# Kernel tuning notes

Measured on AMD Instinct MI355X. Metric: run time of the kernel, lower is better.

The kernel has to match this reference:

```python
import jax, jax.numpy as jnp
import numpy as np

D_MODEL = 1024
N_HEADS = 16
HEAD_DIM = D_MODEL // N_HEADS
B, L = 2, 2048


def setup_inputs() -> dict:
    key = jax.random.key(0)
    ks = jax.random.split(key, 11)
    s = 1.0 / np.sqrt(D_MODEL)
    inp = {
        'query': jax.random.normal(ks[0], (B, L, D_MODEL), dtype=jnp.float32),
        'key': jax.random.normal(ks[1], (B, L, D_MODEL), dtype=jnp.float32),
        'value': jax.random.normal(ks[2], (B, L, D_MODEL), dtype=jnp.float32),
        'Wq_w': jax.random.normal(ks[3], (D_MODEL, D_MODEL), dtype=jnp.float32) * s,
        'Wq_b': jnp.zeros((D_MODEL,), dtype=jnp.float32),
        'Wk_w': jax.random.normal(ks[4], (D_MODEL, D_MODEL), dtype=jnp.float32) * s,
        'Wk_b': jnp.zeros((D_MODEL,), dtype=jnp.float32),
        'Wv_w': jax.random.normal(ks[5], (D_MODEL, D_MODEL), dtype=jnp.float32) * s,
        'Wv_b': jnp.zeros((D_MODEL,), dtype=jnp.float32),
        'Wo_w': jax.random.normal(ks[6], (D_MODEL, D_MODEL), dtype=jnp.float32) * s,
        'Wo_b': jnp.zeros((D_MODEL,), dtype=jnp.float32),
    }
    return inp


def reference(query, key, value, Wq_w, Wq_b, Wk_w, Wk_b, Wv_w, Wv_b, Wo_w, Wo_b):
    b = query.shape[0]
    # torch Linear: y = x @ W^T + b
    Q = query @ Wq_w.T + Wq_b
    K = key @ Wk_w.T + Wk_b
    V = value @ Wv_w.T + Wv_b
    # [B, L, D] -> [B, H, L, hd]
    def split_heads(x):
        return x.reshape(b, -1, N_HEADS, HEAD_DIM).transpose(0, 2, 1, 3)
    Qh, Kh, Vh = split_heads(Q), split_heads(K), split_heads(V)
    scale = 1.0 / jnp.sqrt(jnp.float32(HEAD_DIM))
    # energy: [B, H, Lq, Lk]
    energy = jnp.einsum('bhqd,bhkd->bhqk', Qh, Kh) * scale
    # NOTE: original code applies softmax over dim=1 (the HEADS axis) — faithful reproduction
    attn = jax.nn.softmax(energy, axis=1)
    out = jnp.einsum('bhqk,bhkd->bhqd', attn, Vh)  # [B, H, Lq, hd]
    out = out.transpose(0, 2, 1, 3).reshape(b, -1, D_MODEL)
    return out @ Wo_w.T + Wo_b
```

## Files before the change

kernel.cpp:

```cpp
#include <hip/hip_runtime.h>
#include <hip/hip_bf16.h>
#include <hip/hip_fp16.h>

#define DM 1024
#define NH 16
#define HD 64
#define LL 2048

typedef __attribute__((ext_vector_type(8))) short bf16x8;
typedef __attribute__((ext_vector_type(4))) float f32x4;

#define MFMA16(a,b,c) __builtin_amdgcn_mfma_f32_16x16x32_bf16((a),(b),(c),0,0,0)

#define GL16(g, l) __builtin_amdgcn_global_load_lds( \
    (const __attribute__((address_space(1))) unsigned int*)(g), \
    (__attribute__((address_space(3))) unsigned int*)(l), 16, 0, 0)

__device__ __forceinline__ ushort f2bf(float f) {
  union { float f; unsigned int u; } v; v.f = f;
  unsigned int u = v.u + 0x7fffu + ((v.u >> 16) & 1u);
  return (ushort)(u >> 16);
}

__global__ __launch_bounds__(256) void cvt7(const float* __restrict__ s0, ushort* __restrict__ d0, int n0,
                                            const float* __restrict__ s1, ushort* __restrict__ d1, int n1,
                                            const float* __restrict__ s2, ushort* __restrict__ d2, int n2,
                                            const float* __restrict__ s3, ushort* __restrict__ d3, int n3,
                                            const float* __restrict__ s4, ushort* __restrict__ d4, int n4,
                                            const float* __restrict__ s5, ushort* __restrict__ d5, int n5,
                                            const float* __restrict__ s6, ushort* __restrict__ d6, int n6) {
  int i = (blockIdx.x * 256 + threadIdx.x) * 4;
  const float* s; ushort* d;
  if (i < n0) { s = s0; d = d0; }
  else if ((i -= n0) < n1) { s = s1; d = d1; }
  else if ((i -= n1) < n2) { s = s2; d = d2; }
  else if ((i -= n2) < n3) { s = s3; d = d3; }
  else if ((i -= n3) < n4) { s = s4; d = d4; }
  else if ((i -= n4) < n5) { s = s5; d = d5; }
  else if ((i -= n5) < n6) { s = s6; d = d6; }
  else return;
  float4 v = *(const float4*)(s + i);
  union { ushort u[4]; unsigned long long ll; } o;
  o.u[0] = f2bf(v.x); o.u[1] = f2bf(v.y); o.u[2] = f2bf(v.z); o.u[3] = f2bf(v.w);
  *(unsigned long long*)(d + i) = o.ll;
}

__global__ __launch_bounds__(256) void gemm_qkv(const ushort* __restrict__ qA, const ushort* __restrict__ qW,
                                                const float* __restrict__ qb, ushort* __restrict__ qO,
                                                const ushort* __restrict__ kA, const ushort* __restrict__ kW,
                                                const float* __restrict__ kb, ushort* __restrict__ kO,
                                                const ushort* __restrict__ vA, const ushort* __restrict__ vW,
                                                const float* __restrict__ vb, ushort* __restrict__ vO) {
  __shared__ ushort lA[2][128][64];
  __shared__ ushort lB[2][128][64];
  const int z = blockIdx.z;
  const ushort* Ab; const ushort* Wb; const float* bias; ushort* outp;
  float alpha; bool trans;
  if (z == 0)      { Ab = qA; Wb = qW; bias = qb; outp = qO; alpha = 0.125f; trans = false; }
  else if (z == 1) { Ab = kA; Wb = kW; bias = kb; outp = kO; alpha = 1.0f;   trans = false; }
  else             { Ab = vA; Wb = vW; bias = vb; outp = vO; alpha = 1.0f;   trans = true;  }

  const int m0 = blockIdx.x * 128, n0 = blockIdx.y * 128;
  const int t = threadIdx.x;
  const int w = t >> 6, lane = t & 63, lr = lane & 15, lg = lane >> 4;
  const int wm = (w >> 1) * 64, wn = (w & 1) * 64;
  const int lrow8 = lane >> 3;
  const int scol = ((lane & 7) ^ lrow8) * 8;

  f32x4 acc[4][4];
  #pragma unroll
  for (int i = 0; i < 4; ++i)
    #pragma unroll
    for (int j = 0; j < 4; ++j) acc[i][j] = (f32x4){0.f, 0.f, 0.f, 0.f};

  #pragma unroll
  for (int c = 0; c < 4; ++c) {
    GL16(Ab + (m0 + w * 32 + c * 8 + lrow8) * DM + scol, &lA[0][w * 32 + c * 8][0]);
    GL16(Wb + (n0 + w * 32 + c * 8 + lrow8) * DM + scol, &lB[0][w * 32 + c * 8][0]);
  }
  __syncthreads();

  int cur = 0;
  for (int k0 = 0; k0 < DM; k0 += 64) {
    if (k0 + 64 < DM) {
      #pragma unroll
      for (int c = 0; c < 4; ++c) {
        GL16(Ab + (m0 + w * 32 + c * 8 + lrow8) * DM + k0 + 64 + scol, &lA[cur ^ 1][w * 32 + c * 8][0]);
        GL16(Wb + (n0 + w * 32 + c * 8 + lrow8) * DM + k0 + 64 + scol, &lB[cur ^ 1][w * 32 + c * 8][0]);
      }
    }
    #pragma unroll
    for (int ks = 0; ks < 2; ++ks) {
      bf16x8 aF[4], bF[4];
      #pragma unroll
      for (int i = 0; i < 4; ++i)
        aF[i] = *(const bf16x8*)&lA[cur][wm + i * 16 + lr][(((ks * 4 + lg) ^ (lr & 7)) * 8)];
      #pragma unroll
      for (int j = 0; j < 4; ++j)
        bF[j] = *(const bf16x8*)&lB[cur][wn + j * 16 + lr][(((ks * 4 + lg) ^ (lr & 7)) * 8)];
      #pragma unroll
      for (int i = 0; i < 4; ++i)
        #pragma unroll
        for (int j = 0; j < 4; ++j)
          acc[i][j] = MFMA16(aF[i], bF[j], acc[i][j]);
    }
    __syncthreads();
    cur ^= 1;
  }

  #pragma unroll
  for (int i = 0; i < 4; ++i)
    #pragma unroll
    for (int j = 0; j < 4; ++j)
      #pragma unroll
      for (int r = 0; r < 4; ++r) {
        int m = m0 + wm + i * 16 + lg * 4 + r;
        int n = n0 + wn + j * 16 + lr;
        float v = (acc[i][j][r] + bias[n]) * alpha;
        int b = m >> 11, q = m & 2047, h = n >> 6, d = n & 63;
        if (!trans)
          outp[((b * NH + h) * LL + q) * HD + d] = f2bf(v);
        else
          outp[((b * NH + h) * HD + d) * LL + q] = f2bf(v);
      }
}

__global__ __launch_bounds__(256) void gemm_out(const ushort* __restrict__ Ab,
                                                const ushort* __restrict__ Wb,
                                                const float* __restrict__ bias,
                                                float* __restrict__ outf) {
  __shared__ ushort lA[2][64][64];
  __shared__ ushort lB[2][128][64];
  const int m0 = blockIdx.x * 64, n0 = blockIdx.y * 128;
  const int t = threadIdx.x;
  const int w = t >> 6, lane = t & 63, lr = lane & 15, lg = lane >> 4;
  const int wm = (w >> 1) * 32, wn = (w & 1) * 64;
  const int lrow8 = lane >> 3;
  const int scol = ((lane & 7) ^ lrow8) * 8;

  f32x4 acc[2][4];
  #pragma unroll
  for (int i = 0; i < 2; ++i)
    #pragma unroll
    for (int j = 0; j < 4; ++j) acc[i][j] = (f32x4){0.f, 0.f, 0.f, 0.f};

  #pragma unroll
  for (int c = 0; c < 2; ++c)
    GL16(Ab + (m0 + w * 16 + c * 8 + lrow8) * DM + scol, &lA[0][w * 16 + c * 8][0]);
  #pragma unroll
  for (int c = 0; c < 4; ++c)
    GL16(Wb + (n0 + w * 32 + c * 8 + lrow8) * DM + scol, &lB[0][w * 32 + c * 8][0]);
  __syncthreads();

  int cur = 0;
  for (int k0 = 0; k0 < DM; k0 += 64) {
    if (k0 + 64 < DM) {
      #pragma unroll
      for (int c = 0; c < 2; ++c)
        GL16(Ab + (m0 + w * 16 + c * 8 + lrow8) * DM + k0 + 64 + scol, &lA[cur ^ 1][w * 16 + c * 8][0]);
      #pragma unroll
      for (int c = 0; c < 4; ++c)
        GL16(Wb + (n0 + w * 32 + c * 8 + lrow8) * DM + k0 + 64 + scol, &lB[cur ^ 1][w * 32 + c * 8][0]);
    }
    #pragma unroll
    for (int ks = 0; ks < 2; ++ks) {
      bf16x8 aF[2], bF[4];
      #pragma unroll
      for (int i = 0; i < 2; ++i)
        aF[i] = *(const bf16x8*)&lA[cur][wm + i * 16 + lr][(((ks * 4 + lg) ^ (lr & 7)) * 8)];
      #pragma unroll
      for (int j = 0; j < 4; ++j)
        bF[j] = *(const bf16x8*)&lB[cur][wn + j * 16 + lr][(((ks * 4 + lg) ^ (lr & 7)) * 8)];
      #pragma unroll
      for (int i = 0; i < 2; ++i)
        #pragma unroll
        for (int j = 0; j < 4; ++j)
          acc[i][j] = MFMA16(aF[i], bF[j], acc[i][j]);
    }
    __syncthreads();
    cur ^= 1;
  }

  #pragma unroll
  for (int i = 0; i < 2; ++i)
    #pragma unroll
    for (int j = 0; j < 4; ++j)
      #pragma unroll
      for (int r = 0; r < 4; ++r) {
        int m = m0 + wm + i * 16 + lg * 4 + r;
        int n = n0 + wn + j * 16 + lr;
        outf[m * DM + n] = acc[i][j][r] + bias[n];
      }
}

__global__ __launch_bounds__(256) void pass_a_m(const ushort* __restrict__ Qh,
                                                const ushort* __restrict__ Kh,
                                                __half* __restrict__ rdenH) {
  __shared__ ushort lQ[2][128][64];
  __shared__ ushort lK[2][128][64];
  const int b = blockIdx.z, q0 = blockIdx.y * 128, k0 = blockIdx.x * 128;
  const int t = threadIdx.x, w = t >> 6, lane = t & 63, lr = lane & 15, lg = lane >> 4;
  const int lrow8 = lane >> 3;
  const int scol = ((lane & 7) ^ lrow8) * 8;

  f32x4 acc[2][8];
  #pragma unroll
  for (int i = 0; i < 2; ++i)
    #pragma unroll
    for (int j = 0; j < 8; ++j) acc[i][j] = (f32x4){0.f, 0.f, 0.f, 0.f};

  #pragma unroll
  for (int c = 0; c < 4; ++c) {
    GL16(Qh + ((b * NH) * LL + q0 + w * 32 + c * 8 + lrow8) * HD + scol, &lQ[0][w * 32 + c * 8][0]);
    GL16(Kh + ((b * NH) * LL + k0 + w * 32 + c * 8 + lrow8) * HD + scol, &lK[0][w * 32 + c * 8][0]);
  }
  __syncthreads();

  int cur = 0;
  for (int h = 0; h < NH; ++h) {
    if (h + 1 < NH) {
      #pragma unroll
      for (int c = 0; c < 4; ++c) {
        GL16(Qh + ((b * NH + h + 1) * LL + q0 + w * 32 + c * 8 + lrow8) * HD + scol, &lQ[cur ^ 1][w * 32 + c * 8][0]);
        GL16(Kh + ((b * NH + h + 1) * LL + k0 + w * 32 + c * 8 + lrow8) * HD + scol, &lK[cur ^ 1][w * 32 + c * 8][0]);
      }
    }
    #pragma unroll
    for (int i = 0; i < 2; ++i) {
      int qrow = w * 32 + i * 16 + lr;
      bf16x8 a0 = *(const bf16x8*)&lQ[cur][qrow][((lg ^ (lr & 7)) * 8)];
      bf16x8 a1 = *(const bf16x8*)&lQ[cur][qrow][(((4 + lg) ^ (lr & 7)) * 8)];
      #pragma unroll
      for (int j = 0; j < 8; ++j) {
        int krow = j * 16 + lr;
        bf16x8 b0 = *(const bf16x8*)&lK[cur][krow][((lg ^ (lr & 7)) * 8)];
        bf16x8 b1 = *(const bf16x8*)&lK[cur][krow][(((4 + lg) ^ (lr & 7)) * 8)];
        f32x4 e = {0.f, 0.f, 0.f, 0.f};
        e = MFMA16(b0, a0, e);
        e = MFMA16(b1, a1, e);
        #pragma unroll
        for (int r = 0; r < 4; ++r) acc[i][j][r] += __expf(e[r]);
      }
    }
    __syncthreads();
    cur ^= 1;
  }

  #pragma unroll
  for (int i = 0; i < 2; ++i)
    #pragma unroll
    for (int j = 0; j < 8; ++j) {
      int q = q0 + w * 32 + i * 16 + lr;
      int k = k0 + j * 16 + lg * 4;
      union { __half2 h2[2]; uint2 u; } pk;
      pk.h2[0] = __floats2half2_rn(__builtin_amdgcn_rcpf(acc[i][j][0]),
                                   __builtin_amdgcn_rcpf(acc[i][j][1]));
      pk.h2[1] = __floats2half2_rn(__builtin_amdgcn_rcpf(acc[i][j][2]),
                                   __builtin_amdgcn_rcpf(acc[i][j][3]));
      *(uint2*)&rdenH[(size_t)(b * LL + q) * LL + k] = pk.u;
    }
}

#define PB_BODY(PH)                                                              \
  {                                                                              \
    const int T = tt + PH;                                                       \
    const int k0 = T * 64;                                                       \
    uint2 rdN[4];                                                                \
    if (T + 1 < 32) {                                                            \
      GL16(Kh + (bh * LL + k0 + 64 + w * 8 + lrow8) * HD + scol,                 \
           &lK[PH ^ 1][w * 8][0]);                                               \
      GL16(Vt + (bh * HD + w * 8 + lrow8) * LL + k0 + 64 + scol,                 \
           &lV[PH ^ 1][w * 8][0]);                                               \
      _Pragma("unroll")                                                          \
      for (int j = 0; j < 4; ++j)                                                \
        rdN[j] = *(const uint2*)(rrow + k0 + 64 + j * 16 + lg * 4);              \
    }                                                                            \
    __builtin_amdgcn_s_setprio(1);                                               \
    if (T > 0) {                                                                 \
      bf16x8 aP0 = *(const bf16x8*)&U.p[w][lr][lg * 8];                          \
      bf16x8 aP1 = *(const bf16x8*)&U.p[w][lr][32 + lg * 8];                     \
      _Pragma("unroll")                                                          \
      for (int j = 0; j < 4; ++j) {                                              \
        accO[j] = MFMA16(aP0, vF0[j], accO[j]);                                  \
        accO[j] = MFMA16(aP1, vF1[j], accO[j]);                                  \
      }                                                                          \
    }                                                                            \
    f32x4 e[4];                                                                  \
    _Pragma("unroll")                                                            \
    for (int j = 0; j < 4; ++j) {                                                \
      int krow = j * 16 + lr;                                                    \
      bf16x8 kf0 = *(const bf16x8*)&lK[PH][krow][((lg ^ (lr & 7)) * 8)];         \
      bf16x8 kf1 = *(const bf16x8*)&lK[PH][krow][(((4 + lg) ^ (lr & 7)) * 8)];   \
      e[j] = (f32x4){0.f, 0.f, 0.f, 0.f};                                        \
      e[j] = MFMA16(kf0, aQ0, e[j]);                                             \
      e[j] = MFMA16(kf1, aQ1, e[j]);                                             \
    }                                                                            \
    __builtin_amdgcn_s_setprio(0);                                               \
    _Pragma("unroll")                                                            \
    for (int j = 0; j < 4; ++j) {                                                \
      int vrow = j * 16 + lr;                                                    \
      vF0[j] = *(const bf16x8*)&lV[PH][vrow][((lg ^ (lr & 7)) * 8)];             \
      vF1[j] = *(const bf16x8*)&lV[PH][vrow][(((4 + lg) ^ (lr & 7)) * 8)];       \
    }                                                                            \
    _Pragma("unroll")                                                            \
    for (int j = 0; j < 4; ++j) {                                                \
      float2 f0 = __half22float2(*reinterpret_cast<const __half2*>(&rdC[j].x));  \
      float2 f1 = __half22float2(*reinterpret_cast<const __half2*>(&rdC[j].y));  \
      union { __hip_bfloat162 b2[2]; uint2 u; } pk;                              \
      pk.b2[0] = __float22bfloat162_rn(make_float2(__expf(e[j][0]) * f0.x,       \
                                                   __expf(e[j][1]) * f0.y));     \
      pk.b2[1] = __float22bfloat162_rn(make_float2(__expf(e[j][2]) * f1.x,       \
                                                   __expf(e[j][3]) * f1.y));     \
      *(uint2*)&U.p[w][lr][j * 16 + lg * 4] = pk.u;                              \
    }                                                                            \
    if (T + 1 < 32) {                                                            \
      _Pragma("unroll")                                                          \
      for (int j = 0; j < 4; ++j) rdC[j] = rdN[j];                               \
    }                                                                            \
    __syncthreads();                                                             \
  }

__global__ __launch_bounds__(512, 4) void pass_b_m(const ushort* __restrict__ Qh,
                                                   const ushort* __restrict__ Kh,
                                                   const ushort* __restrict__ Vt,
                                                   const __half* __restrict__ rdenH,
                                                   ushort* __restrict__ AO) {
  __shared__ union UQP { ushort q[128][64]; ushort p[8][16][72]; } U;
  __shared__ ushort lK[2][64][64];
  __shared__ ushort lV[2][64][64];
  const int fid = blockIdx.x + 16 * (blockIdx.y + NH * blockIdx.z);
  const int nid = (fid & 7) * 64 + (fid >> 3);
  const int q0 = (nid & 15) * 128;
  const int h  = (nid >> 4) & 15;
  const int b  = nid >> 8;
  const int t = threadIdx.x, w = t >> 6, lane = t & 63, lr = lane & 15, lg = lane >> 4;
  const int lrow8 = lane >> 3;
  const int scol = ((lane & 7) ^ lrow8) * 8;
  const int bh = b * NH + h;

  #pragma unroll
  for (int u = 0; u < 2; ++u) {
    int c = u * 512 + t;
    int row = c >> 3, col = (c & 7) * 8;
    *(bf16x8*)&U.q[row][col] = *(const bf16x8*)&Qh[(bh * LL + q0 + row) * HD + col];
  }
  GL16(Kh + (bh * LL + w * 8 + lrow8) * HD + scol, &lK[0][w * 8][0]);
  GL16(Vt + (bh * HD + w * 8 + lrow8) * LL + scol, &lV[0][w * 8][0]);
  const int qg = q0 + w * 16 + lr;
  const __half* rrow = rdenH + (size_t)(b * LL + qg) * LL;
  uint2 rdC[4];
  #pragma unroll
  for (int j = 0; j < 4; ++j) rdC[j] = *(const uint2*)(rrow + j * 16 + lg * 4);
  __syncthreads();

  bf16x8 aQ0 = *(const bf16x8*)&U.q[w * 16 + lr][lg * 8];
  bf16x8 aQ1 = *(const bf16x8*)&U.q[w * 16 + lr][32 + lg * 8];
  __syncthreads();

  f32x4 accO[4];
  #pragma unroll
  for (int j = 0; j < 4; ++j) accO[j] = (f32x4){0.f, 0.f, 0.f, 0.f};
  bf16x8 vF0[4], vF1[4];

  for (int tt = 0; tt < 32; tt += 2) {
    PB_BODY(0)
    PB_BODY(1)
  }

  {
    bf16x8 aP0 = *(const bf16x8*)&U.p[w][lr][lg * 8];
    bf16x8 aP1 = *(const bf16x8*)&U.p[w][lr][32 + lg * 8];
    #pragma unroll
    for (int j = 0; j < 4; ++j) {
      accO[j] = MFMA16(aP0, vF0[j], accO[j]);
      accO[j] = MFMA16(aP1, vF1[j], accO[j]);
    }
  }

  #pragma unroll
  for (int j = 0; j < 4; ++j)
    #pragma unroll
    for (int r = 0; r < 4; ++r) {
      int q = q0 + w * 16 + lg * 4 + r;
      int d = j * 16 + lr;
      AO[(b * LL + q) * DM + h * HD + d] = f2bf(accO[j][r]);
    }
}

extern "C" void kernel_launch(void* const* d_in, const int* in_sizes, int n_in,
                              void* d_out, int out_size, void* d_ws, size_t ws_size,
                              hipStream_t stream) {
  const float* query = (const float*)d_in[0];
  const float* key   = (const float*)d_in[1];
  const float* value = (const float*)d_in[2];
  const float* Wq_w  = (const float*)d_in[3];
  const float* Wq_b  = (const float*)d_in[4];
  const float* Wk_w  = (const float*)d_in[5];
  const float* Wk_b  = (const float*)d_in[6];
  const float* Wv_w  = (const float*)d_in[7];
  const float* Wv_b  = (const float*)d_in[8];
  const float* Wo_w  = (const float*)d_in[9];
  const float* Wo_b  = (const float*)d_in[10];

  char* ws = (char*)d_ws;
  char* dob = (char*)d_out;
  ushort* Qh  = (ushort*)(ws);
  ushort* Kh  = (ushort*)(ws + (8u  << 20));
  ushort* Vt  = (ushort*)(ws + (16u << 20));
  ushort* AO  = (ushort*)(ws + (24u << 20));
  ushort* qbf = (ushort*)(ws + (32u << 20));
  ushort* kbf = (ushort*)(ws + (40u << 20));
  ushort* Wob = (ushort*)(ws + (48u << 20));
  ushort* vbf = (ushort*)(dob);
  ushort* Wqb = (ushort*)(dob + (8u  << 20));
  ushort* Wkb = (ushort*)(dob + (10u << 20));
  ushort* Wvb = (ushort*)(dob + (12u << 20));
  __half* rdn = (__half*)d_out;

  const int NA = 2 * LL * DM;
  const int NW = DM * DM;

  cvt7<<<(3 * NA + 4 * NW) / 1024, 256, 0, stream>>>(
      query, qbf, NA, key, kbf, NA, value, vbf, NA,
      Wq_w, Wqb, NW, Wk_w, Wkb, NW, Wv_w, Wvb, NW, Wo_w, Wob, NW);

  gemm_qkv<<<dim3(32, 8, 3), 256, 0, stream>>>(qbf, Wqb, Wq_b, Qh,
                                               kbf, Wkb, Wk_b, Kh,
                                               vbf, Wvb, Wv_b, Vt);

  pass_a_m<<<dim3(16, 16, 2), 256, 0, stream>>>(Qh, Kh, rdn);
  pass_b_m<<<dim3(16, NH, 2), 512, 0, stream>>>(Qh, Kh, Vt, rdn, AO);

  gemm_out<<<dim3(64, 8), 256, 0, stream>>>(AO, Wob, Wo_b, (float*)d_out);
}
```

Before: 192.2 us.

## Read K/V fragments directly from global memory, dropping LDS double-buffer pipeline

The P·V pass kernel stops staging K and V tiles in LDS through async global_load_lds double buffering with barriers. Each wave now loads its Q, K and V MFMA fragments straight from global memory and relies on cache, keeping LDS only for the per-wave P transpose. This removes the barriers and shared-memory staging, but every wave re-reads the same K/V tiles and loses the prefetch overlap. The occupancy hint in launch_bounds is dropped. The P store and reload now go through LDS without any sync, which is presumably safe only because each wave reads just the rows it wrote itself.

```diff
diff --git a/kernel.cpp b/kernel.cpp
--- a/kernel.cpp
+++ b/kernel.cpp
@@ -261,119 +261,63 @@
     }
 }
 
-#define PB_BODY(PH)                                                              \
-  {                                                                              \
-    const int T = tt + PH;                                                       \
-    const int k0 = T * 64;                                                       \
-    uint2 rdN[4];                                                                \
-    if (T + 1 < 32) {                                                            \
-      GL16(Kh + (bh * LL + k0 + 64 + w * 8 + lrow8) * HD + scol,                 \
-           &lK[PH ^ 1][w * 8][0]);                                               \
-      GL16(Vt + (bh * HD + w * 8 + lrow8) * LL + k0 + 64 + scol,                 \
-           &lV[PH ^ 1][w * 8][0]);                                               \
-      _Pragma("unroll")                                                          \
-      for (int j = 0; j < 4; ++j)                                                \
-        rdN[j] = *(const uint2*)(rrow + k0 + 64 + j * 16 + lg * 4);              \
-    }                                                                            \
-    __builtin_amdgcn_s_setprio(1);                                               \
-    if (T > 0) {                                                                 \
-      bf16x8 aP0 = *(const bf16x8*)&U.p[w][lr][lg * 8];                          \
-      bf16x8 aP1 = *(const bf16x8*)&U.p[w][lr][32 + lg * 8];                     \
-      _Pragma("unroll")                                                          \
-      for (int j = 0; j < 4; ++j) {                                              \
-        accO[j] = MFMA16(aP0, vF0[j], accO[j]);                                  \
-        accO[j] = MFMA16(aP1, vF1[j], accO[j]);                                  \
-      }                                                                          \
-    }                                                                            \
-    f32x4 e[4];                                                                  \
-    _Pragma("unroll")                                                            \
-    for (int j = 0; j < 4; ++j) {                                                \
-      int krow = j * 16 + lr;                                                    \
-      bf16x8 kf0 = *(const bf16x8*)&lK[PH][krow][((lg ^ (lr & 7)) * 8)];         \
-      bf16x8 kf1 = *(const bf16x8*)&lK[PH][krow][(((4 + lg) ^ (lr & 7)) * 8)];   \
-      e[j] = (f32x4){0.f, 0.f, 0.f, 0.f};                                        \
-      e[j] = MFMA16(kf0, aQ0, e[j]);                                             \
-      e[j] = MFMA16(kf1, aQ1, e[j]);                                             \
-    }                                                                            \
-    __builtin_amdgcn_s_setprio(0);                                               \
-    _Pragma("unroll")                                                            \
-    for (int j = 0; j < 4; ++j) {                                                \
-      int vrow = j * 16 + lr;                                                    \
-      vF0[j] = *(const bf16x8*)&lV[PH][vrow][((lg ^ (lr & 7)) * 8)];             \
-      vF1[j] = *(const bf16x8*)&lV[PH][vrow][(((4 + lg) ^ (lr & 7)) * 8)];       \
-    }                                                                            \
-    _Pragma("unroll")                                                            \
-    for (int j = 0; j < 4; ++j) {                                                \
-      float2 f0 = __half22float2(*reinterpret_cast<const __half2*>(&rdC[j].x));  \
-      float2 f1 = __half22float2(*reinterpret_cast<const __half2*>(&rdC[j].y));  \
-      union { __hip_bfloat162 b2[2]; uint2 u; } pk;                              \
-      pk.b2[0] = __float22bfloat162_rn(make_float2(__expf(e[j][0]) * f0.x,       \
-                                                   __expf(e[j][1]) * f0.y));     \
-      pk.b2[1] = __float22bfloat162_rn(make_float2(__expf(e[j][2]) * f1.x,       \
-                                                   __expf(e[j][3]) * f1.y));     \
-      *(uint2*)&U.p[w][lr][j * 16 + lg * 4] = pk.u;                              \
-    }                                                                            \
-    if (T + 1 < 32) {                                                            \
-      _Pragma("unroll")                                                          \
-      for (int j = 0; j < 4; ++j) rdC[j] = rdN[j];                               \
-    }                                                                            \
-    __syncthreads();                                                             \
-  }
-
-__global__ __launch_bounds__(512, 4) void pass_b_m(const ushort* __restrict__ Qh,
-                                                   const ushort* __restrict__ Kh,
-                                                   const ushort* __restrict__ Vt,
-                                                   const __half* __restrict__ rdenH,
-                                                   ushort* __restrict__ AO) {
-  __shared__ union UQP { ushort q[128][64]; ushort p[8][16][72]; } U;
-  __shared__ ushort lK[2][64][64];
-  __shared__ ushort lV[2][64][64];
+__global__ __launch_bounds__(512) void pass_b_m(const ushort* __restrict__ Qh,
+                                                const ushort* __restrict__ Kh,
+                                                const ushort* __restrict__ Vt,
+                                                const __half* __restrict__ rdenH,
+                                                ushort* __restrict__ AO) {
+  __shared__ ushort lP[8][16][72];
   const int fid = blockIdx.x + 16 * (blockIdx.y + NH * blockIdx.z);
   const int nid = (fid & 7) * 64 + (fid >> 3);
   const int q0 = (nid & 15) * 128;
   const int h  = (nid >> 4) & 15;
   const int b  = nid >> 8;
   const int t = threadIdx.x, w = t >> 6, lane = t & 63, lr = lane & 15, lg = lane >> 4;
-  const int lrow8 = lane >> 3;
-  const int scol = ((lane & 7) ^ lrow8) * 8;
   const int bh = b * NH + h;
-
-  #pragma unroll
-  for (int u = 0; u < 2; ++u) {
-    int c = u * 512 + t;
-    int row = c >> 3, col = (c & 7) * 8;
-    *(bf16x8*)&U.q[row][col] = *(const bf16x8*)&Qh[(bh * LL + q0 + row) * HD + col];
-  }
-  GL16(Kh + (bh * LL + w * 8 + lrow8) * HD + scol, &lK[0][w * 8][0]);
-  GL16(Vt + (bh * HD + w * 8 + lrow8) * LL + scol, &lV[0][w * 8][0]);
   const int qg = q0 + w * 16 + lr;
+
+  const ushort* qp = Qh + (size_t)(bh * LL + qg) * HD;
+  bf16x8 aQ0 = *(const bf16x8*)(qp + lg * 8);
+  bf16x8 aQ1 = *(const bf16x8*)(qp + 32 + lg * 8);
+
   const __half* rrow = rdenH + (size_t)(b * LL + qg) * LL;
-  uint2 rdC[4];
-  #pragma unroll
-  for (int j = 0; j < 4; ++j) rdC[j] = *(const uint2*)(rrow + j * 16 + lg * 4);
-  __syncthreads();
-
-  bf16x8 aQ0 = *(const bf16x8*)&U.q[w * 16 + lr][lg * 8];
-  bf16x8 aQ1 = *(const bf16x8*)&U.q[w * 16 + lr][32 + lg * 8];
-  __syncthreads();
 
   f32x4 accO[4];
   #pragma unroll
   for (int j = 0; j < 4; ++j) accO[j] = (f32x4){0.f, 0.f, 0.f, 0.f};
-  bf16x8 vF0[4], vF1[4];
-
-  for (int tt = 0; tt < 32; tt += 2) {
-    PB_BODY(0)
-    PB_BODY(1)
-  }
-
-  {
-    bf16x8 aP0 = *(const bf16x8*)&U.p[w][lr][lg * 8];
-    bf16x8 aP1 = *(const bf16x8*)&U.p[w][lr][32 + lg * 8];
+
+  for (int k0 = 0; k0 < LL; k0 += 64) {
+    f32x4 e[4];
     #pragma unroll
     for (int j = 0; j < 4; ++j) {
-      accO[j] = MFMA16(aP0, vF0[j], accO[j]);
-      accO[j] = MFMA16(aP1, vF1[j], accO[j]);
+      const ushort* kp = Kh + (size_t)(bh * LL + k0 + j * 16 + lr) * HD;
+      bf16x8 kf0 = *(const bf16x8*)(kp + lg * 8);
+      bf16x8 kf1 = *(const bf16x8*)(kp + 32 + lg * 8);
+      e[j] = (f32x4){0.f, 0.f, 0.f, 0.f};
+      e[j] = MFMA16(kf0, aQ0, e[j]);
+      e[j] = MFMA16(kf1, aQ1, e[j]);
+    }
+    #pragma unroll
+    for (int j = 0; j < 4; ++j) {
+      uint2 rd8 = *(const uint2*)(rrow + k0 + j * 16 + lg * 4);
+      float2 f0 = __half22float2(*reinterpret_cast<const __half2*>(&rd8.x));
+      float2 f1 = __half22float2(*reinterpret_cast<const __half2*>(&rd8.y));
+      union { __hip_bfloat162 b2[2]; uint2 u; } pk;
+      pk.b2[0] = __float22bfloat162_rn(make_float2(__expf(e[j][0]) * f0.x,
+                                                   __expf(e[j][1]) * f0.y));
+      pk.b2[1] = __float22bfloat162_rn(make_float2(__expf(e[j][2]) * f1.x,
+                                                   __expf(e[j][3]) * f1.y));
+      *(uint2*)&lP[w][lr][j * 16 + lg * 4] = pk.u;
+    }
+    bf16x8 aP0 = *(const bf16x8*)&lP[w][lr][lg * 8];
+    bf16x8 aP1 = *(const bf16x8*)&lP[w][lr][32 + lg * 8];
+    #pragma unroll
+    for (int j = 0; j < 4; ++j) {
+      const ushort* vp = Vt + (size_t)(bh * HD + j * 16 + lr) * LL + k0;
+      bf16x8 vf0 = *(const bf16x8*)(vp + lg * 8);
+      bf16x8 vf1 = *(const bf16x8*)(vp + 32 + lg * 8);
+      accO[j] = MFMA16(aP0, vf0, accO[j]);
+      accO[j] = MFMA16(aP1, vf1, accO[j]);
     }
   }
 
@@ -383,7 +327,7 @@
     for (int r = 0; r < 4; ++r) {
       int q = q0 + w * 16 + lg * 4 + r;
       int d = j * 16 + lr;
-      AO[(b * LL + q) * DM + h * HD + d] = f2bf(accO[j][r]);
+      AO[(size_t)(b * LL + q) * DM + h * HD + d] = f2bf(accO[j][r]);
     }
 }
 
```

New measurement: 401.5 us. +108.9%, slower.

## Split pass_b key dimension into two halves with fp32 partials and reduction kernel

Applied to the files above, without the earlier changes.

Pass B now splits the key loop across two blocks (split-K), doubling the grid from 512 to 1024 blocks so more CUs stay busy. Each half writes fp32 partial outputs, and a new reduce_half kernel sums them and converts to bf16 for the output projection. This trades extra global traffic (two fp32 partial buffers of 16MB each) and an extra launch for better occupancy and parallelism in the attention pass. Workspace offsets are rearranged so AO reuses the Vt region and Wob moves up.

```diff
diff --git a/kernel.cpp b/kernel.cpp
--- a/kernel.cpp
+++ b/kernel.cpp
@@ -45,6 +45,22 @@
   *(unsigned long long*)(d + i) = o.ll;
 }
 
+__global__ __launch_bounds__(256) void reduce_half(const float* __restrict__ p,
+                                                   ushort* __restrict__ out) {
+  const int HALFN = 2 * LL * DM;
+  int i = (blockIdx.x * 256 + threadIdx.x) * 8;
+  float4 a0 = *(const float4*)(p + i);
+  float4 a1 = *(const float4*)(p + i + 4);
+  float4 b0 = *(const float4*)(p + HALFN + i);
+  float4 b1 = *(const float4*)(p + HALFN + i + 4);
+  union { ushort u[8]; uint4 q; } o;
+  o.u[0] = f2bf(a0.x + b0.x); o.u[1] = f2bf(a0.y + b0.y);
+  o.u[2] = f2bf(a0.z + b0.z); o.u[3] = f2bf(a0.w + b0.w);
+  o.u[4] = f2bf(a1.x + b1.x); o.u[5] = f2bf(a1.y + b1.y);
+  o.u[6] = f2bf(a1.z + b1.z); o.u[7] = f2bf(a1.w + b1.w);
+  *(uint4*)(out + i) = o.q;
+}
+
 __global__ __launch_bounds__(256) void gemm_qkv(const ushort* __restrict__ qA, const ushort* __restrict__ qW,
                                                 const float* __restrict__ qb, ushort* __restrict__ qO,
                                                 const ushort* __restrict__ kA, const ushort* __restrict__ kW,
@@ -264,9 +280,9 @@
 #define PB_BODY(PH)                                                              \
   {                                                                              \
     const int T = tt + PH;                                                       \
-    const int k0 = T * 64;                                                       \
+    const int k0 = kbase + T * 64;                                               \
     uint2 rdN[4];                                                                \
-    if (T + 1 < 32) {                                                            \
+    if (T + 1 < 16) {                                                            \
       GL16(Kh + (bh * LL + k0 + 64 + w * 8 + lrow8) * HD + scol,                 \
            &lK[PH ^ 1][w * 8][0]);                                               \
       GL16(Vt + (bh * HD + w * 8 + lrow8) * LL + k0 + 64 + scol,                 \
@@ -313,26 +329,28 @@
                                                    __expf(e[j][3]) * f1.y));     \
       *(uint2*)&U.p[w][lr][j * 16 + lg * 4] = pk.u;                              \
     }                                                                            \
-    if (T + 1 < 32) {                                                            \
+    if (T + 1 < 16) {                                                            \
       _Pragma("unroll")                                                          \
       for (int j = 0; j < 4; ++j) rdC[j] = rdN[j];                               \
     }                                                                            \
-    __syncthreads();                                                             \
+    if (T < 15) __syncthreads();                                                 \
   }
 
 __global__ __launch_bounds__(512, 4) void pass_b_m(const ushort* __restrict__ Qh,
                                                    const ushort* __restrict__ Kh,
                                                    const ushort* __restrict__ Vt,
                                                    const __half* __restrict__ rdenH,
-                                                   ushort* __restrict__ AO) {
+                                                   float* __restrict__ pP) {
   __shared__ union UQP { ushort q[128][64]; ushort p[8][16][72]; } U;
   __shared__ ushort lK[2][64][64];
   __shared__ ushort lV[2][64][64];
-  const int fid = blockIdx.x + 16 * (blockIdx.y + NH * blockIdx.z);
-  const int nid = (fid & 7) * 64 + (fid >> 3);
-  const int q0 = (nid & 15) * 128;
-  const int h  = (nid >> 4) & 15;
-  const int b  = nid >> 8;
+  const int fid = blockIdx.x + 32 * (blockIdx.y + NH * blockIdx.z);
+  const int nid = (fid & 7) * 128 + (fid >> 3);
+  const int q0   = (nid & 15) * 128;
+  const int half = (nid >> 4) & 1;
+  const int h    = (nid >> 5) & 15;
+  const int b    = nid >> 9;
+  const int kbase = half * 1024;
   const int t = threadIdx.x, w = t >> 6, lane = t & 63, lr = lane & 15, lg = lane >> 4;
   const int lrow8 = lane >> 3;
   const int scol = ((lane & 7) ^ lrow8) * 8;
@@ -344,13 +362,13 @@
     int row = c >> 3, col = (c & 7) * 8;
     *(bf16x8*)&U.q[row][col] = *(const bf16x8*)&Qh[(bh * LL + q0 + row) * HD + col];
   }
-  GL16(Kh + (bh * LL + w * 8 + lrow8) * HD + scol, &lK[0][w * 8][0]);
-  GL16(Vt + (bh * HD + w * 8 + lrow8) * LL + scol, &lV[0][w * 8][0]);
+  GL16(Kh + (bh * LL + kbase + w * 8 + lrow8) * HD + scol, &lK[0][w * 8][0]);
+  GL16(Vt + (bh * HD + w * 8 + lrow8) * LL + kbase + scol, &lV[0][w * 8][0]);
   const int qg = q0 + w * 16 + lr;
   const __half* rrow = rdenH + (size_t)(b * LL + qg) * LL;
   uint2 rdC[4];
   #pragma unroll
-  for (int j = 0; j < 4; ++j) rdC[j] = *(const uint2*)(rrow + j * 16 + lg * 4);
+  for (int j = 0; j < 4; ++j) rdC[j] = *(const uint2*)(rrow + kbase + j * 16 + lg * 4);
   __syncthreads();
 
   bf16x8 aQ0 = *(const bf16x8*)&U.q[w * 16 + lr][lg * 8];
@@ -362,7 +380,7 @@
   for (int j = 0; j < 4; ++j) accO[j] = (f32x4){0.f, 0.f, 0.f, 0.f};
   bf16x8 vF0[4], vF1[4];
 
-  for (int tt = 0; tt < 32; tt += 2) {
+  for (int tt = 0; tt < 16; tt += 2) {
     PB_BODY(0)
     PB_BODY(1)
   }
@@ -377,13 +395,14 @@
     }
   }
 
+  float* po = pP + (size_t)half * (2 * LL * DM);
   #pragma unroll
   for (int j = 0; j < 4; ++j)
     #pragma unroll
     for (int r = 0; r < 4; ++r) {
       int q = q0 + w * 16 + lg * 4 + r;
       int d = j * 16 + lr;
-      AO[(b * LL + q) * DM + h * HD + d] = f2bf(accO[j][r]);
+      po[(size_t)(b * LL + q) * DM + h * HD + d] = accO[j][r];
     }
 }
 
@@ -407,10 +426,11 @@
   ushort* Qh  = (ushort*)(ws);
   ushort* Kh  = (ushort*)(ws + (8u  << 20));
   ushort* Vt  = (ushort*)(ws + (16u << 20));
-  ushort* AO  = (ushort*)(ws + (24u << 20));
+  ushort* AO  = (ushort*)(ws + (16u << 20));
+  float*  pP  = (float*) (ws + (24u << 20));
   ushort* qbf = (ushort*)(ws + (32u << 20));
   ushort* kbf = (ushort*)(ws + (40u << 20));
-  ushort* Wob = (ushort*)(ws + (48u << 20));
+  ushort* Wob = (ushort*)(ws + (56u << 20));
   ushort* vbf = (ushort*)(dob);
   ushort* Wqb = (ushort*)(dob + (8u  << 20));
   ushort* Wkb = (ushort*)(dob + (10u << 20));
@@ -429,7 +449,8 @@
                                                vbf, Wvb, Wv_b, Vt);
 
   pass_a_m<<<dim3(16, 16, 2), 256, 0, stream>>>(Qh, Kh, rdn);
-  pass_b_m<<<dim3(16, NH, 2), 512, 0, stream>>>(Qh, Kh, Vt, rdn, AO);
+  pass_b_m<<<dim3(32, NH, 2), 512, 0, stream>>>(Qh, Kh, Vt, rdn, pP);
+  reduce_half<<<NA / (256 * 8), 256, 0, stream>>>(pP, AO);
 
   gemm_out<<<dim3(64, 8), 256, 0, stream>>>(AO, Wob, Wo_b, (float*)d_out);
 }
```

Result: slower. 203.4 us (+5.8%).
